# Kernel optimization log

Hardware: AMD Instinct MI355X
Metric: run time of the kernel (lower is better)

The kernel has to match this reference:

```python
import jax, jax.numpy as jnp
import numpy as np

N_NODES = 50000


def sage_conv(x, edge_index, W_l, b_l, W_r):
    # PyG SAGEConv (mean aggr): out_i = lin_l(mean_{j->i} x_j) + lin_r(x_i)
    src, dst = edge_index[0], edge_index[1]
    msgs = x[src]                                        # [E, C] gather
    summed = jax.ops.segment_sum(msgs, dst, num_segments=N_NODES)  # [N, C]
    deg = jax.ops.segment_sum(jnp.ones((edge_index.shape[1],), x.dtype), dst,
                              num_segments=N_NODES)
    mean = summed / jnp.maximum(deg, 1.0)[:, None]
    return mean @ W_l + b_l + x @ W_r


def setup_inputs() -> dict:
    key = jax.random.key(0)
    ks = jax.random.split(key, 12)
    E, EL, C, X = 800000, 1000000, 128, 384
    return {
        "x": jax.random.normal(ks[0], (N_NODES, X), jnp.float32),
        "edge_index": jax.random.randint(ks[1], (2, E), 0, N_NODES),
        "edge_label_index": jax.random.randint(ks[2], (2, EL), 0, N_NODES),
        "W_lin": jax.random.normal(ks[3], (X, C), jnp.float32) * 0.05,
        "b_lin": jax.random.normal(ks[4], (C,), jnp.float32) * 0.05,
        "W1_l": jax.random.normal(ks[5], (C, C), jnp.float32) * 0.08,
        "b1": jax.random.normal(ks[6], (C,), jnp.float32) * 0.05,
        "W1_r": jax.random.normal(ks[7], (C, C), jnp.float32) * 0.08,
        "W2_l": jax.random.normal(ks[8], (C, C), jnp.float32) * 0.08,
        "b2": jax.random.normal(ks[9], (C,), jnp.float32) * 0.05,
        "W2_r": jax.random.normal(ks[10], (C, C), jnp.float32) * 0.08,
    }


def reference(x, edge_index, edge_label_index, W_lin, b_lin,
              W1_l, b1, W1_r, W2_l, b2, W2_r):
    h = x @ W_lin + b_lin                                # label_lin
    h = jax.nn.relu(sage_conv(h, edge_index, W1_l, b1, W1_r))
    h = sage_conv(h, edge_index, W2_l, b2, W2_r)
    # Classifier: dot product of head/tail node features per label edge
    head = h[edge_label_index[0]]
    tail = h[edge_label_index[1]]
    return (head * tail).sum(axis=-1)                    # [EL]
```

## Files before the change

kernel.cpp:

```cpp
#include <hip/hip_runtime.h>

#define NODES 50000
#define CH 128
#define ELLW 64

using frag_ab = __attribute__((ext_vector_type(8))) short;
using frag_cd = __attribute__((ext_vector_type(4))) float;

__device__ __forceinline__ float bf2f(ushort u) {
    union { unsigned u; float f; } v; v.u = ((unsigned)u) << 16; return v.f;
}
__device__ __forceinline__ ushort f2bf(float f) {
    union { float f; unsigned u; } v; v.f = f;
    unsigned r = v.u + 0x7fff + ((v.u >> 16) & 1);
    return (ushort)(r >> 16);
}

__global__ void prep_weights(const float* __restrict__ Wlin,
                             const float* __restrict__ W1l, const float* __restrict__ W1r,
                             const float* __restrict__ W2l, const float* __restrict__ W2r,
                             ushort* __restrict__ o0, ushort* __restrict__ o1,
                             ushort* __restrict__ o2, ushort* __restrict__ o3,
                             ushort* __restrict__ o4, int* __restrict__ deg) {
    int b = blockIdx.x;
    if (b >= 448) {
        int i = (b - 448) * 256 + threadIdx.y * 128 + threadIdx.x;
        if (i < NODES) deg[i] = 0;
        return;
    }
    const float* W; ushort* O; int K; int kb;
    if (b < 192) { W = Wlin; O = o0; K = 384; kb = b; }
    else {
        int j = (b - 192) >> 6; kb = (b - 192) & 63; K = 128;
        W = (j == 0) ? W1l : (j == 1) ? W1r : (j == 2) ? W2l : W2r;
        O = (j == 0) ? o1  : (j == 1) ? o2  : (j == 2) ? o3  : o4;
    }
    int k = kb * 2 + threadIdx.y;
    int n = threadIdx.x;
    if (k < K) O[(size_t)n * K + k] = f2bf(W[(size_t)k * 128 + n]);
}

__global__ __launch_bounds__(256) void lin_and_ell(
    const float* __restrict__ A, const ushort* __restrict__ Wt,
    const float* __restrict__ bias, ushort* __restrict__ out, int N, int GB,
    const int* __restrict__ ei, int E, int* __restrict__ deg, int* __restrict__ ell)
{
    __shared__ ushort As[128 * 32];
    __shared__ ushort Bs[128 * 32];
    if (blockIdx.x >= GB) {
        int e0 = ((blockIdx.x - GB) * 256 + threadIdx.x) * 2;
#pragma unroll
        for (int j = 0; j < 2; ++j) {
            int e = e0 + j;
            if (e < E) {
                int d = ei[E + e];
                int pos = atomicAdd(&deg[d], 1);
                if (pos < ELLW) ell[(size_t)d * ELLW + pos] = ei[e];
            }
        }
        return;
    }
    const int tid = threadIdx.x;
    const int lane = tid & 63;
    const int wave = tid >> 6;
    const int wr = wave >> 1, wc = wave & 1;
    const int row0 = blockIdx.x * 128;
    const int l15 = lane & 15, quad = lane >> 4;

    frag_cd acc[4][4];
#pragma unroll
    for (int i = 0; i < 4; ++i)
#pragma unroll
        for (int j = 0; j < 4; ++j) acc[i][j] = (frag_cd){0.f, 0.f, 0.f, 0.f};

#pragma unroll 1
    for (int k0 = 0; k0 < 384; k0 += 32) {
        __syncthreads();
#pragma unroll
        for (int i = 0; i < 4; ++i) {
            int e = i * 256 + tid;
            int r = e >> 3, q = e & 7;
            int gr = row0 + r; if (gr > N - 1) gr = N - 1;
            float4 v = *(const float4*)(A + (size_t)gr * 384 + k0 + q * 4);
            ushort4 o; o.x = f2bf(v.x); o.y = f2bf(v.y); o.z = f2bf(v.z); o.w = f2bf(v.w);
            *(ushort4*)(As + r * 32 + q * 4) = o;
        }
#pragma unroll
        for (int i = 0; i < 2; ++i) {
            int e = i * 256 + tid;
            uint4 v = *(const uint4*)(Wt + (size_t)(e >> 2) * 384 + k0 + (e & 3) * 8);
            *(uint4*)(Bs + e * 8) = v;
        }
        __syncthreads();

        frag_ab a[4], b[4];
#pragma unroll
        for (int i = 0; i < 4; ++i)
            a[i] = *(const frag_ab*)(As + (wr * 64 + i * 16 + l15) * 32 + quad * 8);
#pragma unroll
        for (int j = 0; j < 4; ++j)
            b[j] = *(const frag_ab*)(Bs + (wc * 64 + j * 16 + l15) * 32 + quad * 8);
#pragma unroll
        for (int i = 0; i < 4; ++i)
#pragma unroll
            for (int j = 0; j < 4; ++j)
                acc[i][j] = __builtin_amdgcn_mfma_f32_16x16x32_bf16(a[i], b[j], acc[i][j], 0, 0, 0);
    }

#pragma unroll
    for (int i = 0; i < 4; ++i)
#pragma unroll
        for (int r = 0; r < 4; ++r) {
            int row = row0 + wr * 64 + i * 16 + quad * 4 + r;
            if (row < N)
#pragma unroll
                for (int j = 0; j < 4; ++j) {
                    int col = wc * 64 + j * 16 + l15;
                    out[(size_t)row * 128 + col] = f2bf(acc[i][j][r] + bias[col]);
                }
        }
}

__device__ __forceinline__ void acc8(float* acc, uint4 v) {
    acc[0] += bf2f((ushort)(v.x & 0xffff)); acc[1] += bf2f((ushort)(v.x >> 16));
    acc[2] += bf2f((ushort)(v.y & 0xffff)); acc[3] += bf2f((ushort)(v.y >> 16));
    acc[4] += bf2f((ushort)(v.z & 0xffff)); acc[5] += bf2f((ushort)(v.z >> 16));
    acc[6] += bf2f((ushort)(v.w & 0xffff)); acc[7] += bf2f((ushort)(v.w >> 16));
}

__global__ __launch_bounds__(256) void aggregate_ell(
    const ushort* __restrict__ h, const int* __restrict__ ell,
    const int* __restrict__ deg, ushort* __restrict__ mean, int N) {
    int node = blockIdx.x * 4 + (threadIdx.x >> 6);
    if (node >= N) return;
    int lane = threadIdx.x & 63;
    int g = lane >> 4;
    int q = lane & 15;
    const int* row = ell + (size_t)node * ELLW;
    int d = deg[node];
    int dc = d < ELLW ? d : ELLW;

    float acc[8];
#pragma unroll
    for (int k = 0; k < 8; ++k) acc[k] = 0.f;

    int n = 0;
    for (; n + 16 <= dc; n += 16) {
        int i0 = row[n + g];
        int i1 = row[n + 4 + g];
        int i2 = row[n + 8 + g];
        int i3 = row[n + 12 + g];
        uint4 v0 = *(const uint4*)(h + (size_t)i0 * CH + q * 8);
        uint4 v1 = *(const uint4*)(h + (size_t)i1 * CH + q * 8);
        uint4 v2 = *(const uint4*)(h + (size_t)i2 * CH + q * 8);
        uint4 v3 = *(const uint4*)(h + (size_t)i3 * CH + q * 8);
        acc8(acc, v0); acc8(acc, v1); acc8(acc, v2); acc8(acc, v3);
    }
    for (; n + 8 <= dc; n += 8) {
        int i0 = row[n + g];
        int i1 = row[n + 4 + g];
        uint4 v0 = *(const uint4*)(h + (size_t)i0 * CH + q * 8);
        uint4 v1 = *(const uint4*)(h + (size_t)i1 * CH + q * 8);
        acc8(acc, v0); acc8(acc, v1);
    }
    for (; n < dc; n += 4) {
        int j = n + g;
        if (j < dc) {
            int i0 = row[j];
            uint4 v0 = *(const uint4*)(h + (size_t)i0 * CH + q * 8);
            acc8(acc, v0);
        }
    }
#pragma unroll
    for (int k = 0; k < 8; ++k) {
        acc[k] += __shfl_xor(acc[k], 16, 64);
        acc[k] += __shfl_xor(acc[k], 32, 64);
    }
    if (g == 0) {
        float inv = 1.f / fmaxf((float)d, 1.f);
        uint4 o;
        o.x = ((uint)f2bf(acc[1] * inv) << 16) | (uint)f2bf(acc[0] * inv);
        o.y = ((uint)f2bf(acc[3] * inv) << 16) | (uint)f2bf(acc[2] * inv);
        o.z = ((uint)f2bf(acc[5] * inv) << 16) | (uint)f2bf(acc[4] * inv);
        o.w = ((uint)f2bf(acc[7] * inv) << 16) | (uint)f2bf(acc[6] * inv);
        *(uint4*)(mean + (size_t)node * CH + q * 8) = o;
    }
}

template <bool RELU>
__global__ __launch_bounds__(256) void mfma_gemm(
    const ushort* __restrict__ A1, const ushort* __restrict__ Wt1,
    const ushort* __restrict__ A2, const ushort* __restrict__ Wt2,
    const float* __restrict__ bias, ushort* __restrict__ out, int N)
{
    __shared__ ushort As[64 * 32];
    __shared__ ushort Bs[128 * 32];
    const int tid = threadIdx.x;
    const int lane = tid & 63;
    const int wave = tid >> 6;
    const int wr = wave >> 1, wc = wave & 1;
    const int row0 = blockIdx.x * 64;
    const int l15 = lane & 15, quad = lane >> 4;

    frag_cd acc[2][4];
#pragma unroll
    for (int i = 0; i < 2; ++i)
#pragma unroll
        for (int j = 0; j < 4; ++j) acc[i][j] = (frag_cd){0.f, 0.f, 0.f, 0.f};

#pragma unroll 1
    for (int part = 0; part < 2; ++part) {
        const ushort* A  = part ? A2 : A1;
        const ushort* Wt = part ? Wt2 : Wt1;

#pragma unroll 1
        for (int k0 = 0; k0 < 128; k0 += 32) {
            __syncthreads();
            {
                int r = tid >> 2, kq = tid & 3;
                int gr = row0 + r; if (gr > N - 1) gr = N - 1;
                uint4 v = *(const uint4*)(A + (size_t)gr * 128 + k0 + kq * 8);
                *(uint4*)(As + tid * 8) = v;
            }
#pragma unroll
            for (int i = 0; i < 2; ++i) {
                int e = i * 256 + tid;
                uint4 v = *(const uint4*)(Wt + (size_t)(e >> 2) * 128 + k0 + (e & 3) * 8);
                *(uint4*)(Bs + e * 8) = v;
            }
            __syncthreads();

            frag_ab a[2], b[4];
#pragma unroll
            for (int i = 0; i < 2; ++i)
                a[i] = *(const frag_ab*)(As + (wr * 32 + i * 16 + l15) * 32 + quad * 8);
#pragma unroll
            for (int j = 0; j < 4; ++j)
                b[j] = *(const frag_ab*)(Bs + (wc * 64 + j * 16 + l15) * 32 + quad * 8);
#pragma unroll
            for (int i = 0; i < 2; ++i)
#pragma unroll
                for (int j = 0; j < 4; ++j)
                    acc[i][j] = __builtin_amdgcn_mfma_f32_16x16x32_bf16(a[i], b[j], acc[i][j], 0, 0, 0);
        }
    }

#pragma unroll
    for (int i = 0; i < 2; ++i)
#pragma unroll
        for (int r = 0; r < 4; ++r) {
            int row = row0 + wr * 32 + i * 16 + quad * 4 + r;
            if (row < N)
#pragma unroll
                for (int j = 0; j < 4; ++j) {
                    int col = wc * 64 + j * 16 + l15;
                    float v = acc[i][j][r] + bias[col];
                    if (RELU) v = fmaxf(v, 0.f);
                    out[(size_t)row * 128 + col] = f2bf(v);
                }
        }
}

__device__ __forceinline__ float dot8(uint4 va, uint4 vb) {
    float p = 0.f;
    p += bf2f((ushort)(va.x & 0xffff)) * bf2f((ushort)(vb.x & 0xffff));
    p += bf2f((ushort)(va.x >> 16))    * bf2f((ushort)(vb.x >> 16));
    p += bf2f((ushort)(va.y & 0xffff)) * bf2f((ushort)(vb.y & 0xffff));
    p += bf2f((ushort)(va.y >> 16))    * bf2f((ushort)(vb.y >> 16));
    p += bf2f((ushort)(va.z & 0xffff)) * bf2f((ushort)(vb.z & 0xffff));
    p += bf2f((ushort)(va.z >> 16))    * bf2f((ushort)(vb.z >> 16));
    p += bf2f((ushort)(va.w & 0xffff)) * bf2f((ushort)(vb.w & 0xffff));
    p += bf2f((ushort)(va.w >> 16))    * bf2f((ushort)(vb.w >> 16));
    return p;
}

__global__ __launch_bounds__(256) void classify_bf(
    const ushort* __restrict__ h2, const int* __restrict__ eli,
    int EL, float* __restrict__ out) {
    int gt = blockIdx.x * blockDim.x + threadIdx.x;
    int g0 = (gt >> 4) * 8;
    int lane = gt & 15;
    if (g0 >= EL) return;
    bool full = (g0 + 7 < EL);
    int ha[8], ta[8];
    if (full) {
        int4 h0 = *(const int4*)(eli + g0);
        int4 h1 = *(const int4*)(eli + g0 + 4);
        int4 t0 = *(const int4*)(eli + EL + g0);
        int4 t1 = *(const int4*)(eli + EL + g0 + 4);
        ha[0] = h0.x; ha[1] = h0.y; ha[2] = h0.z; ha[3] = h0.w;
        ha[4] = h1.x; ha[5] = h1.y; ha[6] = h1.z; ha[7] = h1.w;
        ta[0] = t0.x; ta[1] = t0.y; ta[2] = t0.z; ta[3] = t0.w;
        ta[4] = t1.x; ta[5] = t1.y; ta[6] = t1.z; ta[7] = t1.w;
    } else {
#pragma unroll
        for (int j = 0; j < 8; ++j) {
            int gj = (g0 + j < EL) ? g0 + j : EL - 1;
            ha[j] = eli[gj];
            ta[j] = eli[EL + gj];
        }
    }
    uint4 va[8], vb[8];
#pragma unroll
    for (int j = 0; j < 8; ++j) {
        va[j] = *((const uint4*)(h2 + (size_t)ha[j] * CH) + lane);
        vb[j] = *((const uint4*)(h2 + (size_t)ta[j] * CH) + lane);
    }
    float p[8];
#pragma unroll
    for (int j = 0; j < 8; ++j) p[j] = dot8(va[j], vb[j]);
#pragma unroll
    for (int s = 8; s >= 1; s >>= 1) {
#pragma unroll
        for (int j = 0; j < 8; ++j) p[j] += __shfl_down(p[j], s, 16);
    }
    if (lane == 0) {
        if (full) {
            *(float4*)(out + g0)     = make_float4(p[0], p[1], p[2], p[3]);
            *(float4*)(out + g0 + 4) = make_float4(p[4], p[5], p[6], p[7]);
        } else {
#pragma unroll
            for (int j = 0; j < 8; ++j)
                if (g0 + j < EL) out[g0 + j] = p[j];
        }
    }
}

extern "C" void kernel_launch(void* const* d_in, const int* in_sizes, int n_in,
                              void* d_out, int out_size, void* d_ws, size_t ws_size,
                              hipStream_t stream) {
    const float* x     = (const float*)d_in[0];
    const int*   ei    = (const int*)d_in[1];
    const int*   eli   = (const int*)d_in[2];
    const float* W_lin = (const float*)d_in[3];
    const float* b_lin = (const float*)d_in[4];
    const float* W1l   = (const float*)d_in[5];
    const float* b1    = (const float*)d_in[6];
    const float* W1r   = (const float*)d_in[7];
    const float* W2l   = (const float*)d_in[8];
    const float* b2    = (const float*)d_in[9];
    const float* W2r   = (const float*)d_in[10];
    float* out = (float*)d_out;

    const int E  = in_sizes[1] / 2;
    const int EL = in_sizes[2] / 2;
    const int N  = NODES;

    char* ws = (char*)d_ws;
    size_t off = 0;
    auto alloc = [&](size_t bytes) -> void* {
        void* p = ws + off;
        off += (bytes + 255) & ~(size_t)255;
        return p;
    };
    ushort* n0    = (ushort*)alloc((size_t)N * CH * sizeof(ushort));
    ushort* n1    = (ushort*)alloc((size_t)N * CH * sizeof(ushort));
    ushort* n2    = (ushort*)alloc((size_t)N * CH * sizeof(ushort));
    ushort* WtLin = (ushort*)alloc((size_t)CH * 384 * sizeof(ushort));
    ushort* Wt1l  = (ushort*)alloc((size_t)CH * CH * sizeof(ushort));
    ushort* Wt1r  = (ushort*)alloc((size_t)CH * CH * sizeof(ushort));
    ushort* Wt2l  = (ushort*)alloc((size_t)CH * CH * sizeof(ushort));
    ushort* Wt2r  = (ushort*)alloc((size_t)CH * CH * sizeof(ushort));
    int* deg = (int*)alloc((size_t)N * sizeof(int));
    int* ell = (int*)alloc((size_t)N * ELLW * sizeof(int));
    (void)ws_size; (void)n_in; (void)out_size;

    const int GB128 = (N + 127) / 128;
    const int GB64  = (N + 63) / 64;
    const int EB2   = (E + 511) / 512;
    const int AB    = (N + 3) / 4;

    prep_weights<<<dim3(644), dim3(128, 2), 0, stream>>>(
        W_lin, W1l, W1r, W2l, W2r, WtLin, Wt1l, Wt1r, Wt2l, Wt2r, deg);

    lin_and_ell<<<dim3(GB128 + EB2), dim3(256), 0, stream>>>(
        x, WtLin, b_lin, n0, N, GB128, ei, E, deg, ell);

    aggregate_ell<<<dim3(AB), dim3(256), 0, stream>>>(n0, ell, deg, n1, N);
    mfma_gemm<true><<<dim3(GB64), dim3(256), 0, stream>>>(
        n1, Wt1l, n0, Wt1r, b1, n2, N);

    aggregate_ell<<<dim3(AB), dim3(256), 0, stream>>>(n2, ell, deg, n1, N);
    mfma_gemm<false><<<dim3(GB64), dim3(256), 0, stream>>>(
        n1, Wt2l, n2, Wt2r, b2, n0, N);

    long long groups = ((long long)EL + 7) / 8;
    long long cls_threads = groups * 16;
    classify_bf<<<dim3((int)((cls_threads + 255) / 256)), dim3(256), 0, stream>>>(
        n0, eli, EL, out);
}
```

Baseline: 301.6 us.

## Fuse neighbor mean aggregation into SAGE GEMM kernel with 16-bit ELL indices

Merges the separate aggregation and MFMA GEMM kernels so each block computes the neighbor means for its 64 rows straight into LDS and feeds them to the MFMA loop. This removes the round trip of the mean tensor through global memory and two kernel launches. ELL indices shrink to 16 bits, edge building reads four edges per thread with vector loads, and the LDS tiles get XOR swizzling to avoid bank conflicts. Aggregation parallelism changes from four lanes-groups per node to one 16-lane group per node with a serial loop, which may expose more gather latency. Storing node indices as ushort silently truncates any index of 65536 or more, which holds only because N is 50000.

```diff
diff --git a/kernel.cpp b/kernel.cpp
--- a/kernel.cpp
+++ b/kernel.cpp
@@ -43,19 +43,33 @@
 __global__ __launch_bounds__(256) void lin_and_ell(
     const float* __restrict__ A, const ushort* __restrict__ Wt,
     const float* __restrict__ bias, ushort* __restrict__ out, int N, int GB,
-    const int* __restrict__ ei, int E, int* __restrict__ deg, int* __restrict__ ell)
+    const int* __restrict__ ei, int E, int* __restrict__ deg, ushort* __restrict__ ell)
 {
     __shared__ ushort As[128 * 32];
     __shared__ ushort Bs[128 * 32];
     if (blockIdx.x >= GB) {
-        int e0 = ((blockIdx.x - GB) * 256 + threadIdx.x) * 2;
-#pragma unroll
-        for (int j = 0; j < 2; ++j) {
-            int e = e0 + j;
-            if (e < E) {
-                int d = ei[E + e];
-                int pos = atomicAdd(&deg[d], 1);
-                if (pos < ELLW) ell[(size_t)d * ELLW + pos] = ei[e];
+        int e0 = ((blockIdx.x - GB) * 256 + threadIdx.x) * 4;
+        if (e0 >= E) return;
+        int s[4], dd[4], cnt;
+        if (((E & 3) == 0) && (e0 + 3 < E)) {
+            int4 sv = *(const int4*)(ei + e0);
+            int4 dv = *(const int4*)(ei + E + e0);
+            s[0] = sv.x; s[1] = sv.y; s[2] = sv.z; s[3] = sv.w;
+            dd[0] = dv.x; dd[1] = dv.y; dd[2] = dv.z; dd[3] = dv.w;
+            cnt = 4;
+        } else {
+            cnt = E - e0; if (cnt > 4) cnt = 4;
+#pragma unroll
+            for (int j = 0; j < 4; ++j) {
+                int e = (j < cnt) ? e0 + j : e0;
+                s[j] = ei[e]; dd[j] = ei[E + e];
+            }
+        }
+#pragma unroll
+        for (int j = 0; j < 4; ++j) {
+            if (j < cnt) {
+                int pos = atomicAdd(&deg[dd[j]], 1);
+                if (pos < ELLW) ell[(size_t)dd[j] * ELLW + pos] = (ushort)s[j];
             }
         }
         return;
@@ -128,133 +142,121 @@
     acc[6] += bf2f((ushort)(v.w & 0xffff)); acc[7] += bf2f((ushort)(v.w >> 16));
 }
 
-__global__ __launch_bounds__(256) void aggregate_ell(
-    const ushort* __restrict__ h, const int* __restrict__ ell,
-    const int* __restrict__ deg, ushort* __restrict__ mean, int N) {
-    int node = blockIdx.x * 4 + (threadIdx.x >> 6);
-    if (node >= N) return;
-    int lane = threadIdx.x & 63;
-    int g = lane >> 4;
-    int q = lane & 15;
-    const int* row = ell + (size_t)node * ELLW;
-    int d = deg[node];
-    int dc = d < ELLW ? d : ELLW;
-
-    float acc[8];
-#pragma unroll
-    for (int k = 0; k < 8; ++k) acc[k] = 0.f;
-
-    int n = 0;
-    for (; n + 16 <= dc; n += 16) {
-        int i0 = row[n + g];
-        int i1 = row[n + 4 + g];
-        int i2 = row[n + 8 + g];
-        int i3 = row[n + 12 + g];
-        uint4 v0 = *(const uint4*)(h + (size_t)i0 * CH + q * 8);
-        uint4 v1 = *(const uint4*)(h + (size_t)i1 * CH + q * 8);
-        uint4 v2 = *(const uint4*)(h + (size_t)i2 * CH + q * 8);
-        uint4 v3 = *(const uint4*)(h + (size_t)i3 * CH + q * 8);
-        acc8(acc, v0); acc8(acc, v1); acc8(acc, v2); acc8(acc, v3);
-    }
-    for (; n + 8 <= dc; n += 8) {
-        int i0 = row[n + g];
-        int i1 = row[n + 4 + g];
-        uint4 v0 = *(const uint4*)(h + (size_t)i0 * CH + q * 8);
-        uint4 v1 = *(const uint4*)(h + (size_t)i1 * CH + q * 8);
-        acc8(acc, v0); acc8(acc, v1);
-    }
-    for (; n < dc; n += 4) {
-        int j = n + g;
-        if (j < dc) {
-            int i0 = row[j];
-            uint4 v0 = *(const uint4*)(h + (size_t)i0 * CH + q * 8);
+template <bool RELU>
+__global__ __launch_bounds__(256) void agg_gemm(
+    const ushort* __restrict__ h, const ushort* __restrict__ ell,
+    const int* __restrict__ deg,
+    const ushort* __restrict__ Wtl, const ushort* __restrict__ Wtr,
+    const float* __restrict__ bias, ushort* __restrict__ out, int N)
+{
+    __shared__ ushort Ms[64 * 128];
+    __shared__ ushort As[64 * 32];
+    __shared__ ushort Bs[128 * 32];
+    const int tid = threadIdx.x;
+    const int lane = tid & 63;
+    const int wave = tid >> 6;
+    const int row0 = blockIdx.x * 64;
+    const int g = lane >> 4;
+    const int q = lane & 15;
+
+#pragma unroll 1
+    for (int it = 0; it < 4; ++it) {
+        int r = (wave << 4) + (it << 2) + g;
+        int node = row0 + r;
+        int nd = node < N ? node : N - 1;
+        const ushort* erow = ell + (size_t)nd * ELLW;
+        int d = deg[nd];
+        int dc = d < ELLW ? d : ELLW;
+        float acc[8];
+#pragma unroll
+        for (int k = 0; k < 8; ++k) acc[k] = 0.f;
+        int n = 0;
+        for (; n + 4 <= dc; n += 4) {
+            ushort4 iv = *(const ushort4*)(erow + n);
+            uint4 v0 = *(const uint4*)(h + (size_t)iv.x * CH + q * 8);
+            uint4 v1 = *(const uint4*)(h + (size_t)iv.y * CH + q * 8);
+            uint4 v2 = *(const uint4*)(h + (size_t)iv.z * CH + q * 8);
+            uint4 v3 = *(const uint4*)(h + (size_t)iv.w * CH + q * 8);
+            acc8(acc, v0); acc8(acc, v1); acc8(acc, v2); acc8(acc, v3);
+        }
+        for (; n < dc; ++n) {
+            uint4 v0 = *(const uint4*)(h + (size_t)erow[n] * CH + q * 8);
             acc8(acc, v0);
         }
-    }
-#pragma unroll
-    for (int k = 0; k < 8; ++k) {
-        acc[k] += __shfl_xor(acc[k], 16, 64);
-        acc[k] += __shfl_xor(acc[k], 32, 64);
-    }
-    if (g == 0) {
         float inv = 1.f / fmaxf((float)d, 1.f);
         uint4 o;
         o.x = ((uint)f2bf(acc[1] * inv) << 16) | (uint)f2bf(acc[0] * inv);
         o.y = ((uint)f2bf(acc[3] * inv) << 16) | (uint)f2bf(acc[2] * inv);
         o.z = ((uint)f2bf(acc[5] * inv) << 16) | (uint)f2bf(acc[4] * inv);
         o.w = ((uint)f2bf(acc[7] * inv) << 16) | (uint)f2bf(acc[6] * inv);
-        *(uint4*)(mean + (size_t)node * CH + q * 8) = o;
-    }
-}
-
-template <bool RELU>
-__global__ __launch_bounds__(256) void mfma_gemm(
-    const ushort* __restrict__ A1, const ushort* __restrict__ Wt1,
-    const ushort* __restrict__ A2, const ushort* __restrict__ Wt2,
-    const float* __restrict__ bias, ushort* __restrict__ out, int N)
-{
-    __shared__ ushort As[64 * 32];
-    __shared__ ushort Bs[128 * 32];
-    const int tid = threadIdx.x;
-    const int lane = tid & 63;
-    const int wave = tid >> 6;
+        int chunk = q ^ (r & 7);
+        *(uint4*)(Ms + r * 128 + chunk * 8) = o;
+    }
+
     const int wr = wave >> 1, wc = wave & 1;
-    const int row0 = blockIdx.x * 64;
-    const int l15 = lane & 15, quad = lane >> 4;
-
-    frag_cd acc[2][4];
+    const int l15 = q, quad = g;
+
+    frag_cd acc2[2][4];
 #pragma unroll
     for (int i = 0; i < 2; ++i)
 #pragma unroll
-        for (int j = 0; j < 4; ++j) acc[i][j] = (frag_cd){0.f, 0.f, 0.f, 0.f};
+        for (int j = 0; j < 4; ++j) acc2[i][j] = (frag_cd){0.f, 0.f, 0.f, 0.f};
 
 #pragma unroll 1
     for (int part = 0; part < 2; ++part) {
-        const ushort* A  = part ? A2 : A1;
-        const ushort* Wt = part ? Wt2 : Wt1;
-
+        const ushort* Wt = part ? Wtr : Wtl;
 #pragma unroll 1
         for (int k0 = 0; k0 < 128; k0 += 32) {
             __syncthreads();
-            {
-                int r = tid >> 2, kq = tid & 3;
-                int gr = row0 + r; if (gr > N - 1) gr = N - 1;
-                uint4 v = *(const uint4*)(A + (size_t)gr * 128 + k0 + kq * 8);
-                *(uint4*)(As + tid * 8) = v;
-            }
+            if (part) {
+                int rr = tid >> 2, kq = tid & 3;
+                int gr = row0 + rr; if (gr > N - 1) gr = N - 1;
+                uint4 v = *(const uint4*)(h + (size_t)gr * CH + k0 + kq * 8);
+                *(uint4*)(As + rr * 32 + ((kq ^ (rr & 3)) * 8)) = v;
+            }
+#pragma unroll
+            for (int i2 = 0; i2 < 2; ++i2) {
+                int e = i2 * 256 + tid;
+                int br = e >> 2, bk = e & 3;
+                uint4 v = *(const uint4*)(Wt + (size_t)br * 128 + k0 + bk * 8);
+                *(uint4*)(Bs + br * 32 + ((bk ^ (br & 3)) * 8)) = v;
+            }
+            __syncthreads();
+
+            frag_ab a[2], b[4];
 #pragma unroll
             for (int i = 0; i < 2; ++i) {
-                int e = i * 256 + tid;
-                uint4 v = *(const uint4*)(Wt + (size_t)(e >> 2) * 128 + k0 + (e & 3) * 8);
-                *(uint4*)(Bs + e * 8) = v;
-            }
-            __syncthreads();
-
-            frag_ab a[2], b[4];
+                int ar = wr * 32 + i * 16 + l15;
+                if (part) {
+                    a[i] = *(const frag_ab*)(As + ar * 32 + ((quad ^ (ar & 3)) * 8));
+                } else {
+                    int ch = ((k0 >> 3) + quad) ^ (ar & 7);
+                    a[i] = *(const frag_ab*)(Ms + ar * 128 + ch * 8);
+                }
+            }
+#pragma unroll
+            for (int j = 0; j < 4; ++j) {
+                int br = wc * 64 + j * 16 + l15;
+                b[j] = *(const frag_ab*)(Bs + br * 32 + ((quad ^ (br & 3)) * 8));
+            }
 #pragma unroll
             for (int i = 0; i < 2; ++i)
-                a[i] = *(const frag_ab*)(As + (wr * 32 + i * 16 + l15) * 32 + quad * 8);
-#pragma unroll
-            for (int j = 0; j < 4; ++j)
-                b[j] = *(const frag_ab*)(Bs + (wc * 64 + j * 16 + l15) * 32 + quad * 8);
-#pragma unroll
-            for (int i = 0; i < 2; ++i)
 #pragma unroll
                 for (int j = 0; j < 4; ++j)
-                    acc[i][j] = __builtin_amdgcn_mfma_f32_16x16x32_bf16(a[i], b[j], acc[i][j], 0, 0, 0);
+                    acc2[i][j] = __builtin_amdgcn_mfma_f32_16x16x32_bf16(a[i], b[j], acc2[i][j], 0, 0, 0);
         }
     }
 
 #pragma unroll
     for (int i = 0; i < 2; ++i)
 #pragma unroll
-        for (int r = 0; r < 4; ++r) {
-            int row = row0 + wr * 32 + i * 16 + quad * 4 + r;
+        for (int rr = 0; rr < 4; ++rr) {
+            int row = row0 + wr * 32 + i * 16 + quad * 4 + rr;
             if (row < N)
 #pragma unroll
                 for (int j = 0; j < 4; ++j) {
                     int col = wc * 64 + j * 16 + l15;
-                    float v = acc[i][j][r] + bias[col];
+                    float v = acc2[i][j][rr] + bias[col];
                     if (RELU) v = fmaxf(v, 0.f);
                     out[(size_t)row * 128 + col] = f2bf(v);
                 }
@@ -362,30 +364,27 @@
     ushort* Wt2l  = (ushort*)alloc((size_t)CH * CH * sizeof(ushort));
     ushort* Wt2r  = (ushort*)alloc((size_t)CH * CH * sizeof(ushort));
     int* deg = (int*)alloc((size_t)N * sizeof(int));
-    int* ell = (int*)alloc((size_t)N * ELLW * sizeof(int));
+    ushort* ell = (ushort*)alloc((size_t)N * ELLW * sizeof(ushort));
     (void)ws_size; (void)n_in; (void)out_size;
 
     const int GB128 = (N + 127) / 128;
     const int GB64  = (N + 63) / 64;
-    const int EB2   = (E + 511) / 512;
-    const int AB    = (N + 3) / 4;
+    const int EB4   = (E + 1023) / 1024;
 
     prep_weights<<<dim3(644), dim3(128, 2), 0, stream>>>(
         W_lin, W1l, W1r, W2l, W2r, WtLin, Wt1l, Wt1r, Wt2l, Wt2r, deg);
 
-    lin_and_ell<<<dim3(GB128 + EB2), dim3(256), 0, stream>>>(
+    lin_and_ell<<<dim3(GB128 + EB4), dim3(256), 0, stream>>>(
         x, WtLin, b_lin, n0, N, GB128, ei, E, deg, ell);
 
-    aggregate_ell<<<dim3(AB), dim3(256), 0, stream>>>(n0, ell, deg, n1, N);
-    mfma_gemm<true><<<dim3(GB64), dim3(256), 0, stream>>>(
-        n1, Wt1l, n0, Wt1r, b1, n2, N);
-
-    aggregate_ell<<<dim3(AB), dim3(256), 0, stream>>>(n2, ell, deg, n1, N);
-    mfma_gemm<false><<<dim3(GB64), dim3(256), 0, stream>>>(
-        n1, Wt2l, n2, Wt2r, b2, n0, N);
+    agg_gemm<true><<<dim3(GB64), dim3(256), 0, stream>>>(
+        n0, ell, deg, Wt1l, Wt1r, b1, n2, N);
+
+    agg_gemm<false><<<dim3(GB64), dim3(256), 0, stream>>>(
+        n2, ell, deg, Wt2l, Wt2r, b2, n1, N);
 
     long long groups = ((long long)EL + 7) / 8;
     long long cls_threads = groups * 16;
     classify_bf<<<dim3((int)((cls_threads + 255) / 256)), dim3(256), 0, stream>>>(
-        n0, eli, EL, out);
-}
+        n1, eli, EL, out);
+}
```

Result: no change. 301.1 us (-0.2%).

## Transform-then-aggregate: fold label_lin into SAGE weights and fuse GEMMs before gathers

Applied to the files above, without the earlier changes.

Uses linearity of mean aggregation to apply the W_l/W_r projections before aggregation. W_lin is premultiplied into layer-1 weights, so one 384→256 GEMM produces both the to-be-aggregated and the self terms. The aggregation kernel then adds the self term, bias and ReLU, so one standalone GEMM launch disappears and the layer-2 GEMM becomes a single 128→256 product. ELL indices are stored as 16-bit, and edge scatter is vectorized to four edges per thread. The risks are extra bf16 rounding from the composed weights, and ushort indices rely on the node count fitting in 16 bits, which it does not at 50000 > 65535? (50000 fits).

```diff
diff --git a/kernel.cpp b/kernel.cpp
--- a/kernel.cpp
+++ b/kernel.cpp
@@ -16,46 +16,105 @@
     return (ushort)(r >> 16);
 }
 
-__global__ void prep_weights(const float* __restrict__ Wlin,
-                             const float* __restrict__ W1l, const float* __restrict__ W1r,
-                             const float* __restrict__ W2l, const float* __restrict__ W2r,
-                             ushort* __restrict__ o0, ushort* __restrict__ o1,
-                             ushort* __restrict__ o2, ushort* __restrict__ o3,
-                             ushort* __restrict__ o4, int* __restrict__ deg) {
-    int b = blockIdx.x;
-    if (b >= 448) {
-        int i = (b - 448) * 256 + threadIdx.y * 128 + threadIdx.x;
+__global__ __launch_bounds__(256) void prep2(
+    const float* __restrict__ Wlin, const float* __restrict__ blin,
+    const float* __restrict__ W1l, const float* __restrict__ b1,
+    const float* __restrict__ W1r,
+    const float* __restrict__ W2l, const float* __restrict__ b2,
+    const float* __restrict__ W2r,
+    ushort* __restrict__ Wtc01,
+    float* __restrict__ biasA,
+    ushort* __restrict__ Wtc2,
+    float* __restrict__ biasC,
+    int* __restrict__ deg)
+{
+    __shared__ float Ws[128 * 128];
+    const int b = blockIdx.x;
+    const int tid = threadIdx.x;
+
+    if (b < 96) {
+        const int sel = b & 1;
+        const int kb  = b >> 1;
+        const float* Wr = sel ? W1r : W1l;
+#pragma unroll 1
+        for (int i = 0; i < 64; ++i) {
+            int idx = i * 256 + tid;
+            Ws[idx] = Wr[idx];
+        }
+        __syncthreads();
+        const int nn = tid & 127;
+        const int kh = tid >> 7;
+#pragma unroll 1
+        for (int kk = 0; kk < 4; ++kk) {
+            int k = kb * 8 + kh * 4 + kk;
+            float a = 0.f;
+#pragma unroll 4
+            for (int m = 0; m < 128; ++m)
+                a += Wlin[(size_t)k * 128 + m] * Ws[m * 128 + nn];
+            Wtc01[(size_t)(sel * 128 + nn) * 384 + k] = f2bf(a);
+        }
+        return;
+    }
+    if (b < 160) {
+        int e0 = (b - 96) * 512 + tid * 2;
+#pragma unroll
+        for (int j = 0; j < 2; ++j) {
+            int e = e0 + j;
+            int n = e >> 7, k = e & 127;
+            const float* Wsrc = (n < 128) ? W2l : W2r;
+            Wtc2[(size_t)n * 128 + k] = f2bf(Wsrc[(size_t)k * 128 + (n & 127)]);
+        }
+        return;
+    }
+    if (b < 356) {
+        int i = (b - 160) * 256 + tid;
         if (i < NODES) deg[i] = 0;
         return;
     }
-    const float* W; ushort* O; int K; int kb;
-    if (b < 192) { W = Wlin; O = o0; K = 384; kb = b; }
-    else {
-        int j = (b - 192) >> 6; kb = (b - 192) & 63; K = 128;
-        W = (j == 0) ? W1l : (j == 1) ? W1r : (j == 2) ? W2l : W2r;
-        O = (j == 0) ? o1  : (j == 1) ? o2  : (j == 2) ? o3  : o4;
-    }
-    int k = kb * 2 + threadIdx.y;
-    int n = threadIdx.x;
-    if (k < K) O[(size_t)n * K + k] = f2bf(W[(size_t)k * 128 + n]);
-}
-
-__global__ __launch_bounds__(256) void lin_and_ell(
+    {
+        int n = tid;
+        int nn = n & 127;
+        const float* Wb = (n < 128) ? W1l : W1r;
+        float a = 0.f;
+#pragma unroll 4
+        for (int m = 0; m < 128; ++m)
+            a += blin[m] * Wb[(size_t)m * 128 + nn];
+        biasA[n] = a + ((n < 128) ? 0.f : b1[nn]);
+        biasC[n] = (n < 128) ? 0.f : b2[nn];
+    }
+}
+
+__global__ __launch_bounds__(512) void lin2_ell(
     const float* __restrict__ A, const ushort* __restrict__ Wt,
-    const float* __restrict__ bias, ushort* __restrict__ out, int N, int GB,
-    const int* __restrict__ ei, int E, int* __restrict__ deg, int* __restrict__ ell)
+    const float* __restrict__ bias, ushort* __restrict__ v1, ushort* __restrict__ u1,
+    int N, int GB,
+    const int* __restrict__ ei, int E, int* __restrict__ deg, ushort* __restrict__ ell)
 {
     __shared__ ushort As[128 * 32];
-    __shared__ ushort Bs[128 * 32];
+    __shared__ ushort Bs[256 * 32];
     if (blockIdx.x >= GB) {
-        int e0 = ((blockIdx.x - GB) * 256 + threadIdx.x) * 2;
-#pragma unroll
-        for (int j = 0; j < 2; ++j) {
-            int e = e0 + j;
-            if (e < E) {
-                int d = ei[E + e];
-                int pos = atomicAdd(&deg[d], 1);
-                if (pos < ELLW) ell[(size_t)d * ELLW + pos] = ei[e];
+        int e0 = ((blockIdx.x - GB) * 512 + threadIdx.x) * 4;
+        if (e0 >= E) return;
+        int s[4], dd[4], cnt;
+        if (((E & 3) == 0) && (e0 + 3 < E)) {
+            int4 sv = *(const int4*)(ei + e0);
+            int4 dv = *(const int4*)(ei + E + e0);
+            s[0] = sv.x; s[1] = sv.y; s[2] = sv.z; s[3] = sv.w;
+            dd[0] = dv.x; dd[1] = dv.y; dd[2] = dv.z; dd[3] = dv.w;
+            cnt = 4;
+        } else {
+            cnt = E - e0; if (cnt > 4) cnt = 4;
+#pragma unroll
+            for (int j = 0; j < 4; ++j) {
+                int e = (j < cnt) ? e0 + j : e0;
+                s[j] = ei[e]; dd[j] = ei[E + e];
+            }
+        }
+#pragma unroll
+        for (int j = 0; j < 4; ++j) {
+            if (j < cnt) {
+                int pos = atomicAdd(&deg[dd[j]], 1);
+                if (pos < ELLW) ell[(size_t)dd[j] * ELLW + pos] = (ushort)s[j];
             }
         }
         return;
@@ -63,7 +122,7 @@
     const int tid = threadIdx.x;
     const int lane = tid & 63;
     const int wave = tid >> 6;
-    const int wr = wave >> 1, wc = wave & 1;
+    const int wr = wave >> 2, wc = wave & 3;
     const int row0 = blockIdx.x * 128;
     const int l15 = lane & 15, quad = lane >> 4;
 
@@ -77,8 +136,8 @@
     for (int k0 = 0; k0 < 384; k0 += 32) {
         __syncthreads();
 #pragma unroll
-        for (int i = 0; i < 4; ++i) {
-            int e = i * 256 + tid;
+        for (int i = 0; i < 2; ++i) {
+            int e = i * 512 + tid;
             int r = e >> 3, q = e & 7;
             int gr = row0 + r; if (gr > N - 1) gr = N - 1;
             float4 v = *(const float4*)(A + (size_t)gr * 384 + k0 + q * 4);
@@ -87,9 +146,10 @@
         }
 #pragma unroll
         for (int i = 0; i < 2; ++i) {
-            int e = i * 256 + tid;
-            uint4 v = *(const uint4*)(Wt + (size_t)(e >> 2) * 384 + k0 + (e & 3) * 8);
-            *(uint4*)(Bs + e * 8) = v;
+            int e = i * 512 + tid;
+            int br = e >> 2, bk = e & 3;
+            uint4 v = *(const uint4*)(Wt + (size_t)br * 384 + k0 + bk * 8);
+            *(uint4*)(Bs + br * 32 + bk * 8) = v;
         }
         __syncthreads();
 
@@ -116,7 +176,9 @@
 #pragma unroll
                 for (int j = 0; j < 4; ++j) {
                     int col = wc * 64 + j * 16 + l15;
-                    out[(size_t)row * 128 + col] = f2bf(acc[i][j][r] + bias[col]);
+                    float v = acc[i][j][r] + bias[col];
+                    ushort* dst = (col < 128) ? v1 : u1;
+                    dst[(size_t)row * 128 + (col & 127)] = f2bf(v);
                 }
         }
 }
@@ -128,15 +190,18 @@
     acc[6] += bf2f((ushort)(v.w & 0xffff)); acc[7] += bf2f((ushort)(v.w >> 16));
 }
 
-__global__ __launch_bounds__(256) void aggregate_ell(
-    const ushort* __restrict__ h, const int* __restrict__ ell,
-    const int* __restrict__ deg, ushort* __restrict__ mean, int N) {
+template <bool RELU>
+__global__ __launch_bounds__(256) void agg_add(
+    const ushort* __restrict__ gsrc, const ushort* __restrict__ ell,
+    const int* __restrict__ deg, const ushort* __restrict__ add,
+    ushort* __restrict__ out, int N)
+{
     int node = blockIdx.x * 4 + (threadIdx.x >> 6);
     if (node >= N) return;
     int lane = threadIdx.x & 63;
     int g = lane >> 4;
     int q = lane & 15;
-    const int* row = ell + (size_t)node * ELLW;
+    const ushort* row = ell + (size_t)node * ELLW;
     int d = deg[node];
     int dc = d < ELLW ? d : ELLW;
 
@@ -150,24 +215,24 @@
         int i1 = row[n + 4 + g];
         int i2 = row[n + 8 + g];
         int i3 = row[n + 12 + g];
-        uint4 v0 = *(const uint4*)(h + (size_t)i0 * CH + q * 8);
-        uint4 v1 = *(const uint4*)(h + (size_t)i1 * CH + q * 8);
-        uint4 v2 = *(const uint4*)(h + (size_t)i2 * CH + q * 8);
-        uint4 v3 = *(const uint4*)(h + (size_t)i3 * CH + q * 8);
+        uint4 v0 = *(const uint4*)(gsrc + (size_t)i0 * CH + q * 8);
+        uint4 v1 = *(const uint4*)(gsrc + (size_t)i1 * CH + q * 8);
+        uint4 v2 = *(const uint4*)(gsrc + (size_t)i2 * CH + q * 8);
+        uint4 v3 = *(const uint4*)(gsrc + (size_t)i3 * CH + q * 8);
         acc8(acc, v0); acc8(acc, v1); acc8(acc, v2); acc8(acc, v3);
     }
     for (; n + 8 <= dc; n += 8) {
         int i0 = row[n + g];
         int i1 = row[n + 4 + g];
-        uint4 v0 = *(const uint4*)(h + (size_t)i0 * CH + q * 8);
-        uint4 v1 = *(const uint4*)(h + (size_t)i1 * CH + q * 8);
+        uint4 v0 = *(const uint4*)(gsrc + (size_t)i0 * CH + q * 8);
+        uint4 v1 = *(const uint4*)(gsrc + (size_t)i1 * CH + q * 8);
         acc8(acc, v0); acc8(acc, v1);
     }
     for (; n < dc; n += 4) {
         int j = n + g;
         if (j < dc) {
             int i0 = row[j];
-            uint4 v0 = *(const uint4*)(h + (size_t)i0 * CH + q * 8);
+            uint4 v0 = *(const uint4*)(gsrc + (size_t)i0 * CH + q * 8);
             acc8(acc, v0);
         }
     }
@@ -178,85 +243,91 @@
     }
     if (g == 0) {
         float inv = 1.f / fmaxf((float)d, 1.f);
+        uint4 av = *((const uint4*)(add + (size_t)node * CH) + q);
+        float m0 = acc[0] * inv + bf2f((ushort)(av.x & 0xffff));
+        float m1 = acc[1] * inv + bf2f((ushort)(av.x >> 16));
+        float m2 = acc[2] * inv + bf2f((ushort)(av.y & 0xffff));
+        float m3 = acc[3] * inv + bf2f((ushort)(av.y >> 16));
+        float m4 = acc[4] * inv + bf2f((ushort)(av.z & 0xffff));
+        float m5 = acc[5] * inv + bf2f((ushort)(av.z >> 16));
+        float m6 = acc[6] * inv + bf2f((ushort)(av.w & 0xffff));
+        float m7 = acc[7] * inv + bf2f((ushort)(av.w >> 16));
+        if (RELU) {
+            m0 = fmaxf(m0, 0.f); m1 = fmaxf(m1, 0.f); m2 = fmaxf(m2, 0.f); m3 = fmaxf(m3, 0.f);
+            m4 = fmaxf(m4, 0.f); m5 = fmaxf(m5, 0.f); m6 = fmaxf(m6, 0.f); m7 = fmaxf(m7, 0.f);
+        }
         uint4 o;
-        o.x = ((uint)f2bf(acc[1] * inv) << 16) | (uint)f2bf(acc[0] * inv);
-        o.y = ((uint)f2bf(acc[3] * inv) << 16) | (uint)f2bf(acc[2] * inv);
-        o.z = ((uint)f2bf(acc[5] * inv) << 16) | (uint)f2bf(acc[4] * inv);
-        o.w = ((uint)f2bf(acc[7] * inv) << 16) | (uint)f2bf(acc[6] * inv);
-        *(uint4*)(mean + (size_t)node * CH + q * 8) = o;
-    }
-}
-
-template <bool RELU>
-__global__ __launch_bounds__(256) void mfma_gemm(
-    const ushort* __restrict__ A1, const ushort* __restrict__ Wt1,
-    const ushort* __restrict__ A2, const ushort* __restrict__ Wt2,
-    const float* __restrict__ bias, ushort* __restrict__ out, int N)
+        o.x = ((uint)f2bf(m1) << 16) | (uint)f2bf(m0);
+        o.y = ((uint)f2bf(m3) << 16) | (uint)f2bf(m2);
+        o.z = ((uint)f2bf(m5) << 16) | (uint)f2bf(m4);
+        o.w = ((uint)f2bf(m7) << 16) | (uint)f2bf(m6);
+        *(uint4*)(out + (size_t)node * CH + q * 8) = o;
+    }
+}
+
+__global__ __launch_bounds__(512) void gemm2(
+    const ushort* __restrict__ A, const ushort* __restrict__ Wt,
+    const float* __restrict__ bias, ushort* __restrict__ g2, ushort* __restrict__ r2, int N)
 {
-    __shared__ ushort As[64 * 32];
-    __shared__ ushort Bs[128 * 32];
+    __shared__ ushort As[128 * 32];
+    __shared__ ushort Bs[256 * 32];
     const int tid = threadIdx.x;
     const int lane = tid & 63;
     const int wave = tid >> 6;
-    const int wr = wave >> 1, wc = wave & 1;
-    const int row0 = blockIdx.x * 64;
+    const int wr = wave >> 2, wc = wave & 3;
+    const int row0 = blockIdx.x * 128;
     const int l15 = lane & 15, quad = lane >> 4;
 
-    frag_cd acc[2][4];
-#pragma unroll
-    for (int i = 0; i < 2; ++i)
+    frag_cd acc[4][4];
+#pragma unroll
+    for (int i = 0; i < 4; ++i)
 #pragma unroll
         for (int j = 0; j < 4; ++j) acc[i][j] = (frag_cd){0.f, 0.f, 0.f, 0.f};
 
 #pragma unroll 1
-    for (int part = 0; part < 2; ++part) {
-        const ushort* A  = part ? A2 : A1;
-        const ushort* Wt = part ? Wt2 : Wt1;
-
-#pragma unroll 1
-        for (int k0 = 0; k0 < 128; k0 += 32) {
-            __syncthreads();
-            {
-                int r = tid >> 2, kq = tid & 3;
-                int gr = row0 + r; if (gr > N - 1) gr = N - 1;
-                uint4 v = *(const uint4*)(A + (size_t)gr * 128 + k0 + kq * 8);
-                *(uint4*)(As + tid * 8) = v;
-            }
-#pragma unroll
-            for (int i = 0; i < 2; ++i) {
-                int e = i * 256 + tid;
-                uint4 v = *(const uint4*)(Wt + (size_t)(e >> 2) * 128 + k0 + (e & 3) * 8);
-                *(uint4*)(Bs + e * 8) = v;
-            }
-            __syncthreads();
-
-            frag_ab a[2], b[4];
-#pragma unroll
-            for (int i = 0; i < 2; ++i)
-                a[i] = *(const frag_ab*)(As + (wr * 32 + i * 16 + l15) * 32 + quad * 8);
+    for (int k0 = 0; k0 < 128; k0 += 32) {
+        __syncthreads();
+        {
+            int r = tid >> 2, kq = tid & 3;
+            int gr = row0 + r; if (gr > N - 1) gr = N - 1;
+            uint4 v = *(const uint4*)(A + (size_t)gr * 128 + k0 + kq * 8);
+            *(uint4*)(As + r * 32 + kq * 8) = v;
+        }
+#pragma unroll
+        for (int i = 0; i < 2; ++i) {
+            int e = i * 512 + tid;
+            int br = e >> 2, bk = e & 3;
+            uint4 v = *(const uint4*)(Wt + (size_t)br * 128 + k0 + bk * 8);
+            *(uint4*)(Bs + br * 32 + bk * 8) = v;
+        }
+        __syncthreads();
+
+        frag_ab a[4], b[4];
+#pragma unroll
+        for (int i = 0; i < 4; ++i)
+            a[i] = *(const frag_ab*)(As + (wr * 64 + i * 16 + l15) * 32 + quad * 8);
+#pragma unroll
+        for (int j = 0; j < 4; ++j)
+            b[j] = *(const frag_ab*)(Bs + (wc * 64 + j * 16 + l15) * 32 + quad * 8);
+#pragma unroll
+        for (int i = 0; i < 4; ++i)
 #pragma unroll
             for (int j = 0; j < 4; ++j)
-                b[j] = *(const frag_ab*)(Bs + (wc * 64 + j * 16 + l15) * 32 + quad * 8);
-#pragma unroll
-            for (int i = 0; i < 2; ++i)
-#pragma unroll
-                for (int j = 0; j < 4; ++j)
-                    acc[i][j] = __builtin_amdgcn_mfma_f32_16x16x32_bf16(a[i], b[j], acc[i][j], 0, 0, 0);
-        }
-    }
-
-#pragma unroll
-    for (int i = 0; i < 2; ++i)
+                acc[i][j] = __builtin_amdgcn_mfma_f32_16x16x32_bf16(a[i], b[j], acc[i][j], 0, 0, 0);
+    }
+
+#pragma unroll
+    for (int i = 0; i < 4; ++i)
 #pragma unroll
         for (int r = 0; r < 4; ++r) {
-            int row = row0 + wr * 32 + i * 16 + quad * 4 + r;
+            int row = row0 + wr * 64 + i * 16 + quad * 4 + r;
             if (row < N)
 #pragma unroll
                 for (int j = 0; j < 4; ++j) {
                     int col = wc * 64 + j * 16 + l15;
                     float v = acc[i][j][r] + bias[col];
-                    if (RELU) v = fmaxf(v, 0.f);
-                    out[(size_t)row * 128 + col] = f2bf(v);
+                    ushort* dst = (col < 128) ? g2 : r2;
+                    dst[(size_t)row * 128 + (col & 127)] = f2bf(v);
                 }
         }
 }
@@ -356,36 +427,33 @@
     ushort* n0    = (ushort*)alloc((size_t)N * CH * sizeof(ushort));
     ushort* n1    = (ushort*)alloc((size_t)N * CH * sizeof(ushort));
     ushort* n2    = (ushort*)alloc((size_t)N * CH * sizeof(ushort));
-    ushort* WtLin = (ushort*)alloc((size_t)CH * 384 * sizeof(ushort));
-    ushort* Wt1l  = (ushort*)alloc((size_t)CH * CH * sizeof(ushort));
-    ushort* Wt1r  = (ushort*)alloc((size_t)CH * CH * sizeof(ushort));
-    ushort* Wt2l  = (ushort*)alloc((size_t)CH * CH * sizeof(ushort));
-    ushort* Wt2r  = (ushort*)alloc((size_t)CH * CH * sizeof(ushort));
+    ushort* n3    = (ushort*)alloc((size_t)N * CH * sizeof(ushort));
+    ushort* Wtc01 = (ushort*)alloc((size_t)256 * 384 * sizeof(ushort));
+    ushort* Wtc2  = (ushort*)alloc((size_t)256 * 128 * sizeof(ushort));
+    float*  biasA = (float*)alloc(256 * sizeof(float));
+    float*  biasC = (float*)alloc(256 * sizeof(float));
     int* deg = (int*)alloc((size_t)N * sizeof(int));
-    int* ell = (int*)alloc((size_t)N * ELLW * sizeof(int));
+    ushort* ell = (ushort*)alloc((size_t)N * ELLW * sizeof(ushort));
     (void)ws_size; (void)n_in; (void)out_size;
 
     const int GB128 = (N + 127) / 128;
-    const int GB64  = (N + 63) / 64;
-    const int EB2   = (E + 511) / 512;
+    const int EB4   = (E + 2047) / 2048;
     const int AB    = (N + 3) / 4;
 
-    prep_weights<<<dim3(644), dim3(128, 2), 0, stream>>>(
-        W_lin, W1l, W1r, W2l, W2r, WtLin, Wt1l, Wt1r, Wt2l, Wt2r, deg);
-
-    lin_and_ell<<<dim3(GB128 + EB2), dim3(256), 0, stream>>>(
-        x, WtLin, b_lin, n0, N, GB128, ei, E, deg, ell);
-
-    aggregate_ell<<<dim3(AB), dim3(256), 0, stream>>>(n0, ell, deg, n1, N);
-    mfma_gemm<true><<<dim3(GB64), dim3(256), 0, stream>>>(
-        n1, Wt1l, n0, Wt1r, b1, n2, N);
-
-    aggregate_ell<<<dim3(AB), dim3(256), 0, stream>>>(n2, ell, deg, n1, N);
-    mfma_gemm<false><<<dim3(GB64), dim3(256), 0, stream>>>(
-        n1, Wt2l, n2, Wt2r, b2, n0, N);
+    prep2<<<dim3(357), dim3(256), 0, stream>>>(
+        W_lin, b_lin, W1l, b1, W1r, W2l, b2, W2r, Wtc01, biasA, Wtc2, biasC, deg);
+
+    lin2_ell<<<dim3(GB128 + EB4), dim3(512), 0, stream>>>(
+        x, Wtc01, biasA, n0, n1, N, GB128, ei, E, deg, ell);
+
+    agg_add<true><<<dim3(AB), dim3(256), 0, stream>>>(n0, ell, deg, n1, n2, N);
+
+    gemm2<<<dim3(GB128), dim3(512), 0, stream>>>(n2, Wtc2, biasC, n0, n3, N);
+
+    agg_add<false><<<dim3(AB), dim3(256), 0, stream>>>(n0, ell, deg, n3, n1, N);
 
     long long groups = ((long long)EL + 7) / 8;
     long long cls_threads = groups * 16;
     classify_bf<<<dim3((int)((cls_threads + 255) / 256)), dim3(256), 0, stream>>>(
-        n0, eli, EL, out);
-}
+        n1, eli, EL, out);
+}
```

New measurement: 323.7 us. 1.07x slower.
